# Kernel optimization log

Measured on AMD Instinct MI355X. Metric: run time of the kernel, lower is better.

Reference implementation:

```python
import jax, jax.numpy as jnp
import numpy as np

N_NODES = 20000
N_EDGES = 640000
D_IN = 128
D_OUT = 128


def setup_inputs() -> dict:
    key = jax.random.key(0)
    k1, k2, k3, k4 = jax.random.split(key, 4)
    x = jax.random.normal(k1, (N_NODES, D_IN), dtype=jnp.float32)
    edge_index = jax.random.randint(k2, (2, N_EDGES), 0, N_NODES, dtype=jnp.int64)
    edge_weight = jnp.ones((N_EDGES,), dtype=jnp.float32)
    # Linear(in_feats, out_feats) params (PyTorch convention: W [out, in])
    bound = 1.0 / np.sqrt(D_IN)
    W = jax.random.uniform(k3, (D_OUT, D_IN), minval=-bound, maxval=bound, dtype=jnp.float32)
    b = jax.random.uniform(k4, (D_OUT,), minval=-bound, maxval=bound, dtype=jnp.float32)
    return {"x": x, "edge_index": edge_index, "edge_weight": edge_weight, "W": W, "b": b}


def reference(x, edge_index, edge_weight, W, b):
    # MeanAggregator: h = Linear(x); out = row-normalized spmm(adj, h)
    h = x @ W.T + b  # [N, D_OUT]
    row, col = edge_index[0], edge_index[1]
    # message = w_ij * h[j], scattered into row i  (spmm with COO adjacency)
    msg = h[col] * edge_weight[:, None]  # [E, D_OUT]
    agg = jax.ops.segment_sum(msg, row, num_segments=N_NODES)  # [N, D_OUT]
    deg = jax.ops.segment_sum(edge_weight, row, num_segments=N_NODES)  # [N]
    deg_inv = jnp.where(deg > 0, 1.0 / deg, 0.0)
    out = agg * deg_inv[:, None]
    # normalize=True -> F.normalize(out, p=2, dim=-1)
    norm = jnp.linalg.norm(out, axis=-1, keepdims=True)
    out = out / jnp.maximum(norm, 1e-12)
    return out
```

## Files before the change

### kernel.cpp

```cpp
#include <hip/hip_runtime.h>
#include <hip/hip_bf16.h>
#include <math.h>

#define N_NODES 20000
#define N_EDGES 640000
#define D 128

#define BSHIFT 4
#define BNODES 16
#define NB 1250
#define CAP2 768
#define AGG_T 1024
#define NBLK1 160
#define CHUNK 4000
#define GPAD 16
#define CASTBLK 625

#define GROWS 16

typedef __attribute__((ext_vector_type(8))) short bf16x8;
typedef __attribute__((ext_vector_type(4))) float f32x4;

static __device__ __forceinline__ unsigned short f2bf(float f) {
  unsigned u = __float_as_uint(f);
  return (unsigned short)((u + 0x7fffu + ((u >> 16) & 1u)) >> 16);
}
static __device__ __forceinline__ float bflo(unsigned v) {
  return __uint_as_float(v << 16);
}
static __device__ __forceinline__ float bfhi(unsigned v) {
  return __uint_as_float(v & 0xffff0000u);
}

__global__ __launch_bounds__(256) void zero_kernel(int* __restrict__ p, int n) {
  const int i = blockIdx.x * 256 + threadIdx.x;
  if (i < n) p[i] = 0;
}

__global__ __launch_bounds__(AGG_T) void castbin_kernel(
    const float* __restrict__ x, const float* __restrict__ W,
    const int* __restrict__ rows, const int* __restrict__ cols,
    const float* __restrict__ ew,
    unsigned* __restrict__ xb, unsigned* __restrict__ Wb,
    int* __restrict__ gcur, uint2* __restrict__ bins) {
  __shared__ uint2 stage[CHUNK];
  __shared__ int cnt[NB];
  __shared__ int lbase[NB];
  __shared__ int gbase[NB];
  const int tid = threadIdx.x;
  if (blockIdx.x < NBLK1) {
    const int e0 = blockIdx.x * CHUNK;
    for (int i = tid; i < NB; i += AGG_T) cnt[i] = 0;
    __syncthreads();
    const int4* r4 = reinterpret_cast<const int4*>(rows + e0);
    int4 rv;
    const bool own = tid < CHUNK / 4;
    if (own) {
      rv = r4[tid];
      atomicAdd(&cnt[rv.x >> BSHIFT], 1);
      atomicAdd(&cnt[rv.y >> BSHIFT], 1);
      atomicAdd(&cnt[rv.z >> BSHIFT], 1);
      atomicAdd(&cnt[rv.w >> BSHIFT], 1);
    }
    __syncthreads();
    if (tid < 64) {
      int carry = 0;
      for (int c0 = 0; c0 < NB; c0 += 64) {
        const int idx = c0 + tid;
        const int v = (idx < NB) ? cnt[idx] : 0;
        int s = v;
#pragma unroll
        for (int off = 1; off < 64; off <<= 1) {
          const int t = __shfl_up(s, off);
          if (tid >= off) s += t;
        }
        if (idx < NB) lbase[idx] = carry + s - v;
        carry += __shfl(s, 63);
      }
    }
    for (int i = tid; i < NB; i += AGG_T) {
      const int c = cnt[i];
      gbase[i] = c ? atomicAdd(&gcur[i * GPAD], c) : 0;
    }
    __syncthreads();
    for (int i = tid; i < NB; i += AGG_T) cnt[i] = 0;
    __syncthreads();
    if (own) {
      const int4 cv = reinterpret_cast<const int4*>(cols + e0)[tid];
      const float4 wv = reinterpret_cast<const float4*>(ew + e0)[tid];
      const int rr[4] = {rv.x, rv.y, rv.z, rv.w};
      const int cc[4] = {cv.x, cv.y, cv.z, cv.w};
      const float ww[4] = {wv.x, wv.y, wv.z, wv.w};
#pragma unroll
      for (int u = 0; u < 4; ++u) {
        const int b = rr[u] >> BSHIFT;
        const int r = atomicAdd(&cnt[b], 1);
        stage[lbase[b] + r] =
            make_uint2(((unsigned)rr[u] << 16) | (unsigned)cc[u],
                       __float_as_uint(ww[u]));
      }
    }
    __syncthreads();
    for (int i = tid; i < CHUNK; i += AGG_T) {
      const uint2 e = stage[i];
      const int b = (int)(e.x >> 20);
      const int p = gbase[b] + (i - lbase[b]);
      if (p < CAP2) bins[(size_t)b * CAP2 + p] = e;
    }
  } else {
    const int i = (blockIdx.x - NBLK1) * AGG_T + tid;
    {
      const float4 v = *reinterpret_cast<const float4*>(&x[(size_t)i * 4]);
      uint2 o;
      o.x = (unsigned)f2bf(v.x) | ((unsigned)f2bf(v.y) << 16);
      o.y = (unsigned)f2bf(v.z) | ((unsigned)f2bf(v.w) << 16);
      *reinterpret_cast<uint2*>(&xb[(size_t)i * 2]) = o;
    }
    if (i < D * D / 4) {
      const float4 v = *reinterpret_cast<const float4*>(&W[(size_t)i * 4]);
      uint2 o;
      o.x = (unsigned)f2bf(v.x) | ((unsigned)f2bf(v.y) << 16);
      o.y = (unsigned)f2bf(v.z) | ((unsigned)f2bf(v.w) << 16);
      *reinterpret_cast<uint2*>(&Wb[(size_t)i * 2]) = o;
    }
  }
}

__global__ __launch_bounds__(AGG_T, 8) void agg_gemm_kernel(
    const unsigned* __restrict__ xb, const int* __restrict__ gcur,
    const uint2* __restrict__ bins, const unsigned* __restrict__ Wb,
    const float* __restrict__ bias, float* __restrict__ out) {
  __shared__ uint2 list[CAP2];
  __shared__ unsigned aggls[BNODES * 64];
  __shared__ int cnt[BNODES];
  __shared__ int base[BNODES];
  __shared__ float degls[BNODES];
  const int b = blockIdx.x;
  const int tid = threadIdx.x;
  const int n = min(gcur[b * GPAD], CAP2);
  if (tid < BNODES) cnt[tid] = 0;
  __syncthreads();

  uint2 ev;
  int rk = -1, rl = 0;
  if (tid < n) {
    ev = bins[(size_t)b * CAP2 + tid];
    rl = (int)(ev.x >> 16) & 15;
    rk = atomicAdd(&cnt[rl], 1);
  }
  __syncthreads();
  if (tid < 64) {
    const int c = (tid < BNODES) ? cnt[tid] : 0;
    int s = c;
#pragma unroll
    for (int off = 1; off < BNODES; off <<= 1) {
      const int t = __shfl_up(s, off);
      if (tid >= off) s += t;
    }
    if (tid < BNODES) base[tid] = s - c;
  }
  __syncthreads();
  if (rk >= 0) list[base[rl] + rk] = ev;
  __syncthreads();

  const int wv = tid >> 6, lane = tid & 63;
  const int q4 = lane >> 4, fidx = lane & 15;
  {
    const int s = base[wv];
    const int ke = s + cnt[wv];
    float a[8] = {0.f, 0.f, 0.f, 0.f, 0.f, 0.f, 0.f, 0.f};
    float dw = 0.f;
    for (int k = s; k < ke; k += 32) {
      uint4 v[8];
      float w[8];
#pragma unroll
      for (int u = 0; u < 8; ++u) {
        int idx = k + u * 4 + q4;
        const bool ok = idx < ke;
        if (!ok) idx = ke - 1;
        const uint2 e = list[idx];
        w[u] = ok ? __uint_as_float(e.y) : 0.f;
        v[u] = *reinterpret_cast<const uint4*>(
            &xb[(size_t)(e.x & 0xffffu) * (D / 2) + fidx * 4]);
      }
#pragma unroll
      for (int u = 0; u < 8; ++u) {
        a[0] += bflo(v[u].x) * w[u]; a[1] += bfhi(v[u].x) * w[u];
        a[2] += bflo(v[u].y) * w[u]; a[3] += bfhi(v[u].y) * w[u];
        a[4] += bflo(v[u].z) * w[u]; a[5] += bfhi(v[u].z) * w[u];
        a[6] += bflo(v[u].w) * w[u]; a[7] += bfhi(v[u].w) * w[u];
        dw += w[u];
      }
    }
#pragma unroll
    for (int j = 0; j < 8; ++j) {
      a[j] += __shfl_xor(a[j], 16);
      a[j] += __shfl_xor(a[j], 32);
    }
    dw += __shfl_xor(dw, 16);
    dw += __shfl_xor(dw, 32);
    const float dinv = dw > 0.f ? 1.f / dw : 0.f;
    if (lane == 0) degls[wv] = dw;
    if (q4 == 0) {
      uint4 o;
      o.x = (unsigned)f2bf(a[0] * dinv) | ((unsigned)f2bf(a[1] * dinv) << 16);
      o.y = (unsigned)f2bf(a[2] * dinv) | ((unsigned)f2bf(a[3] * dinv) << 16);
      o.z = (unsigned)f2bf(a[4] * dinv) | ((unsigned)f2bf(a[5] * dinv) << 16);
      o.w = (unsigned)f2bf(a[6] * dinv) | ((unsigned)f2bf(a[7] * dinv) << 16);
      *reinterpret_cast<uint4*>(
          &aggls[wv * 64 + ((fidx * 4) ^ ((wv & 7) << 2))]) = o;
    }
  }
  __syncthreads();

  if (wv != 0) return;
  const int arow = lane & 15;
  const int koff = (lane >> 4) * 4;

  bf16x8 afr[4];
#pragma unroll
  for (int kk = 0; kk < 4; ++kk) {
    const int wbase = (kk * 16 + koff) ^ ((arow & 7) << 2);
    union { uint4 u; bf16x8 v; } cv;
    cv.u = *reinterpret_cast<const uint4*>(&aggls[arow * 64 + wbase]);
    afr[kk] = cv.v;
  }

  f32x4 acc[8];
#pragma unroll
  for (int t = 0; t < 8; ++t) {
    const int o = t * 16 + (lane & 15);
    f32x4 c = {0.f, 0.f, 0.f, 0.f};
#pragma unroll
    for (int kk = 0; kk < 4; ++kk) {
      union { uint4 u; bf16x8 v; } cv;
      cv.u = *reinterpret_cast<const uint4*>(
          &Wb[(size_t)o * (D / 2) + kk * 16 + koff]);
      c = __builtin_amdgcn_mfma_f32_16x16x32_bf16(afr[kk], cv.v, c, 0, 0, 0);
    }
    acc[t] = c;
  }

  float ss[4] = {0.f, 0.f, 0.f, 0.f};
#pragma unroll
  for (int t = 0; t < 8; ++t) {
    const float bc = bias[t * 16 + (lane & 15)];
#pragma unroll
    for (int r = 0; r < 4; ++r) {
      const float y = acc[t][r] + bc;
      acc[t][r] = y;
      ss[r] += y * y;
    }
  }
#pragma unroll
  for (int r = 0; r < 4; ++r) {
#pragma unroll
    for (int off = 1; off < 16; off <<= 1)
      ss[r] += __shfl_xor(ss[r], off);
  }
  const int row0 = b * BNODES;
  float scale[4];
#pragma unroll
  for (int r = 0; r < 4; ++r) {
    const int lrow = (lane >> 4) * 4 + r;
    const float dw = degls[lrow];
    scale[r] = (dw > 0.f) ? 1.f / fmaxf(sqrtf(ss[r]), 1e-12f) : 0.f;
  }
#pragma unroll
  for (int t = 0; t < 8; ++t) {
#pragma unroll
    for (int r = 0; r < 4; ++r) {
      const int lrow = (lane >> 4) * 4 + r;
      out[(size_t)(row0 + lrow) * D + t * 16 + (lane & 15)] =
          acc[t][r] * scale[r];
    }
  }
}

__global__ __launch_bounds__(256) void scatter_kernel(
    const float* __restrict__ x, const int* __restrict__ rows,
    const int* __restrict__ cols, const float* __restrict__ ew,
    float* __restrict__ out, float* __restrict__ degw) {
  const int e = blockIdx.x * 4 + (threadIdx.x >> 6);
  const int lane = threadIdx.x & 63;
  if (e >= N_EDGES) return;
  const int r = rows[e];
  const int c = cols[e];
  const float w = ew[e];
  const float2 v = *reinterpret_cast<const float2*>(&x[(size_t)c * D + lane * 2]);
  atomicAdd(&out[(size_t)r * D + lane * 2], v.x * w);
  atomicAdd(&out[(size_t)r * D + lane * 2 + 1], v.y * w);
  if (lane == 0) atomicAdd(&degw[r], w);
}

__global__ __launch_bounds__(256) void linear_norm_kernel(
    const float* __restrict__ W, const float* __restrict__ b,
    const float* __restrict__ degw, float* __restrict__ out) {
  __shared__ float Ws[D][D + 1];
  __shared__ float xs[GROWS][D];
  __shared__ float dws[GROWS];
  const int tid = threadIdx.x;
  const int row0 = blockIdx.x * GROWS;
  for (int idx = tid; idx < D * D; idx += 256)
    Ws[idx >> 7][idx & 127] = W[idx];
  if (tid < GROWS) dws[tid] = degw[row0 + tid];
  __syncthreads();
  for (int idx = tid; idx < GROWS * D; idx += 256) {
    const int r = idx >> 7;
    const float dw = dws[r];
    const float dinv = dw > 0.f ? 1.f / dw : 0.f;
    xs[r][idx & 127] = out[(size_t)(row0 + r) * D + (idx & 127)] * dinv;
  }
  __syncthreads();
  const int o = tid & 127;
  const int rh = tid >> 7;
  float acc[GROWS / 2];
#pragma unroll
  for (int j = 0; j < GROWS / 2; ++j) acc[j] = 0.f;
  for (int k = 0; k < D; ++k) {
    const float wv = Ws[o][k];
#pragma unroll
    for (int j = 0; j < GROWS / 2; ++j)
      acc[j] += xs[rh + 2 * j][k] * wv;
  }
  const float bias = b[o];
  __syncthreads();
#pragma unroll
  for (int j = 0; j < GROWS / 2; ++j)
    xs[rh + 2 * j][o] = acc[j] + bias;
  __syncthreads();
  const int w = tid >> 6, lane = tid & 63;
#pragma unroll
  for (int q = 0; q < 4; ++q) {
    const int r = w * 4 + q;
    const float2 v = *reinterpret_cast<const float2*>(&xs[r][lane * 2]);
    float ss = v.x * v.x + v.y * v.y;
#pragma unroll
    for (int off = 1; off < 64; off <<= 1) ss += __shfl_xor(ss, off);
    const float dw = dws[r];
    const float scale = (dw > 0.f) ? 1.f / fmaxf(sqrtf(ss), 1e-12f) : 0.f;
    *reinterpret_cast<float2*>(&out[(size_t)(row0 + r) * D + lane * 2]) =
        make_float2(v.x * scale, v.y * scale);
  }
}

extern "C" void kernel_launch(void* const* d_in, const int* in_sizes, int n_in,
                              void* d_out, int out_size, void* d_ws, size_t ws_size,
                              hipStream_t stream) {
  const float* x  = (const float*)d_in[0];
  const int*   ei = (const int*)d_in[1];
  const float* ew = (const float*)d_in[2];
  const float* W  = (const float*)d_in[3];
  const float* b  = (const float*)d_in[4];
  float* out = (float*)d_out;
  char* ws = (char*)d_ws;

  const int* rows = ei;
  const int* cols = ei + N_EDGES;

  size_t off = 0;
  int* gcur = (int*)(ws + off);        off += (size_t)NB * GPAD * 4;
  float* degw = (float*)(ws + off);    off += (size_t)N_NODES * 4;
  unsigned* xb = (unsigned*)(ws + off);  off += (size_t)N_NODES * (D / 2) * 4;
  unsigned* Wb = (unsigned*)(ws + off);  off += (size_t)D * (D / 2) * 4;
  uint2* bins = (uint2*)(ws + off);    off += (size_t)NB * CAP2 * 8;
  const size_t main_bytes = off;
  const size_t fallback_bytes = (size_t)NB * GPAD * 4 + (size_t)N_NODES * 4;

  if (ws_size >= main_bytes) {
    zero_kernel<<<(NB * GPAD + 255) / 256, 256, 0, stream>>>(gcur, NB * GPAD);
    castbin_kernel<<<NBLK1 + CASTBLK, AGG_T, 0, stream>>>(x, W, rows, cols, ew,
                                                          xb, Wb, gcur, bins);
    agg_gemm_kernel<<<NB, AGG_T, 0, stream>>>(xb, gcur, bins, Wb, b, out);
  } else if (ws_size >= fallback_bytes) {
    hipMemsetAsync(out, 0, (size_t)N_NODES * D * 4, stream);
    hipMemsetAsync(degw, 0, (size_t)N_NODES * 4, stream);
    scatter_kernel<<<(N_EDGES + 3) / 4, 256, 0, stream>>>(x, rows, cols, ew, out, degw);
    linear_norm_kernel<<<N_NODES / GROWS, 256, 0, stream>>>(W, b, degw, out);
  }
}
```

Baseline: 64.27 us.

## Split feature gather into low/high halves across two kernels for cache locality

After: 73.29 us. 14.0% more time.

```diff
diff --git a/kernel.cpp b/kernel.cpp
--- a/kernel.cpp
+++ b/kernel.cpp
@@ -41,7 +41,8 @@
     const float* __restrict__ x, const float* __restrict__ W,
     const int* __restrict__ rows, const int* __restrict__ cols,
     const float* __restrict__ ew,
-    unsigned* __restrict__ xb, unsigned* __restrict__ Wb,
+    unsigned* __restrict__ xb_lo, unsigned* __restrict__ xb_hi,
+    unsigned* __restrict__ Wb,
     int* __restrict__ gcur, uint2* __restrict__ bins) {
   __shared__ uint2 stage[CHUNK];
   __shared__ int cnt[NB];
@@ -110,11 +111,16 @@
   } else {
     const int i = (blockIdx.x - NBLK1) * AGG_T + tid;
     {
+      const int node = i >> 5;
+      const int q = i & 31;
       const float4 v = *reinterpret_cast<const float4*>(&x[(size_t)i * 4]);
       uint2 o;
       o.x = (unsigned)f2bf(v.x) | ((unsigned)f2bf(v.y) << 16);
       o.y = (unsigned)f2bf(v.z) | ((unsigned)f2bf(v.w) << 16);
-      *reinterpret_cast<uint2*>(&xb[(size_t)i * 2]) = o;
+      unsigned* dst = (q < 16)
+          ? &xb_lo[(size_t)node * 32 + q * 2]
+          : &xb_hi[(size_t)node * 32 + (q - 16) * 2];
+      *reinterpret_cast<uint2*>(dst) = o;
     }
     if (i < D * D / 4) {
       const float4 v = *reinterpret_cast<const float4*>(&W[(size_t)i * 4]);
@@ -126,10 +132,93 @@
   }
 }
 
-__global__ __launch_bounds__(AGG_T, 8) void agg_gemm_kernel(
-    const unsigned* __restrict__ xb, const int* __restrict__ gcur,
-    const uint2* __restrict__ bins, const unsigned* __restrict__ Wb,
-    const float* __restrict__ bias, float* __restrict__ out) {
+__global__ __launch_bounds__(AGG_T) void agg_lo_kernel(
+    const unsigned* __restrict__ xb_lo, const int* __restrict__ gcur,
+    const uint2* __restrict__ bins, unsigned* __restrict__ aggb_lo) {
+  __shared__ uint2 list[CAP2];
+  __shared__ int cnt[BNODES];
+  __shared__ int base[BNODES];
+  const int b = blockIdx.x;
+  const int tid = threadIdx.x;
+  const int n = min(gcur[b * GPAD], CAP2);
+  if (tid < BNODES) cnt[tid] = 0;
+  __syncthreads();
+  uint2 ev;
+  int rk = -1, rl = 0;
+  if (tid < n) {
+    ev = bins[(size_t)b * CAP2 + tid];
+    rl = (int)(ev.x >> 16) & 15;
+    rk = atomicAdd(&cnt[rl], 1);
+  }
+  __syncthreads();
+  if (tid < 64) {
+    const int c = (tid < BNODES) ? cnt[tid] : 0;
+    int s = c;
+#pragma unroll
+    for (int off = 1; off < BNODES; off <<= 1) {
+      const int t = __shfl_up(s, off);
+      if (tid >= off) s += t;
+    }
+    if (tid < BNODES) base[tid] = s - c;
+  }
+  __syncthreads();
+  if (rk >= 0) list[base[rl] + rk] = ev;
+  __syncthreads();
+
+  const int wv = tid >> 6, lane = tid & 63;
+  const int o8 = lane >> 3, f = lane & 7;
+  const int s = base[wv];
+  const int ke = s + cnt[wv];
+  float a[8] = {0.f, 0.f, 0.f, 0.f, 0.f, 0.f, 0.f, 0.f};
+  float dw = 0.f;
+  for (int k = s; k < ke; k += 64) {
+    uint4 v[8];
+    float w[8];
+#pragma unroll
+    for (int u = 0; u < 8; ++u) {
+      int idx = k + u * 8 + o8;
+      const bool ok = idx < ke;
+      if (!ok) idx = ke - 1;
+      const uint2 e = list[idx];
+      w[u] = ok ? __uint_as_float(e.y) : 0.f;
+      v[u] = *reinterpret_cast<const uint4*>(
+          &xb_lo[(size_t)(e.x & 0xffffu) * 32 + f * 4]);
+    }
+#pragma unroll
+    for (int u = 0; u < 8; ++u) {
+      a[0] += bflo(v[u].x) * w[u]; a[1] += bfhi(v[u].x) * w[u];
+      a[2] += bflo(v[u].y) * w[u]; a[3] += bfhi(v[u].y) * w[u];
+      a[4] += bflo(v[u].z) * w[u]; a[5] += bfhi(v[u].z) * w[u];
+      a[6] += bflo(v[u].w) * w[u]; a[7] += bfhi(v[u].w) * w[u];
+      dw += w[u];
+    }
+  }
+#pragma unroll
+  for (int j = 0; j < 8; ++j) {
+    a[j] += __shfl_xor(a[j], 8);
+    a[j] += __shfl_xor(a[j], 16);
+    a[j] += __shfl_xor(a[j], 32);
+  }
+  dw += __shfl_xor(dw, 8);
+  dw += __shfl_xor(dw, 16);
+  dw += __shfl_xor(dw, 32);
+  const float dinv = dw > 0.f ? 1.f / dw : 0.f;
+  if (lane < 8) {
+    uint4 o;
+    o.x = (unsigned)f2bf(a[0] * dinv) | ((unsigned)f2bf(a[1] * dinv) << 16);
+    o.y = (unsigned)f2bf(a[2] * dinv) | ((unsigned)f2bf(a[3] * dinv) << 16);
+    o.z = (unsigned)f2bf(a[4] * dinv) | ((unsigned)f2bf(a[5] * dinv) << 16);
+    o.w = (unsigned)f2bf(a[6] * dinv) | ((unsigned)f2bf(a[7] * dinv) << 16);
+    *reinterpret_cast<uint4*>(
+        &aggb_lo[(size_t)(b * BNODES + wv) * 32 + f * 4]) = o;
+  }
+}
+
+__global__ __launch_bounds__(AGG_T) void agg_hi_gemm_kernel(
+    const unsigned* __restrict__ xb_hi, const int* __restrict__ gcur,
+    const uint2* __restrict__ bins, const unsigned* __restrict__ aggb_lo,
+    const unsigned* __restrict__ Wb, const float* __restrict__ bias,
+    float* __restrict__ out) {
   __shared__ uint2 list[CAP2];
   __shared__ unsigned aggls[BNODES * 64];
   __shared__ int cnt[BNODES];
@@ -140,7 +229,6 @@
   const int n = min(gcur[b * GPAD], CAP2);
   if (tid < BNODES) cnt[tid] = 0;
   __syncthreads();
-
   uint2 ev;
   int rk = -1, rl = 0;
   if (tid < n) {
@@ -161,27 +249,34 @@
   }
   __syncthreads();
   if (rk >= 0) list[base[rl] + rk] = ev;
+  if (tid < BNODES * 8) {
+    const int node = tid >> 3, f = tid & 7;
+    const uint4 cv = *reinterpret_cast<const uint4*>(
+        &aggb_lo[(size_t)(b * BNODES + node) * 32 + f * 4]);
+    *reinterpret_cast<uint4*>(
+        &aggls[node * 64 + ((f * 4) ^ ((node & 7) << 2))]) = cv;
+  }
   __syncthreads();
 
   const int wv = tid >> 6, lane = tid & 63;
-  const int q4 = lane >> 4, fidx = lane & 15;
+  const int o8 = lane >> 3, f = lane & 7;
   {
     const int s = base[wv];
     const int ke = s + cnt[wv];
     float a[8] = {0.f, 0.f, 0.f, 0.f, 0.f, 0.f, 0.f, 0.f};
     float dw = 0.f;
-    for (int k = s; k < ke; k += 32) {
+    for (int k = s; k < ke; k += 64) {
       uint4 v[8];
       float w[8];
 #pragma unroll
       for (int u = 0; u < 8; ++u) {
-        int idx = k + u * 4 + q4;
+        int idx = k + u * 8 + o8;
         const bool ok = idx < ke;
         if (!ok) idx = ke - 1;
         const uint2 e = list[idx];
         w[u] = ok ? __uint_as_float(e.y) : 0.f;
         v[u] = *reinterpret_cast<const uint4*>(
-            &xb[(size_t)(e.x & 0xffffu) * (D / 2) + fidx * 4]);
+            &xb_hi[(size_t)(e.x & 0xffffu) * 32 + f * 4]);
       }
 #pragma unroll
       for (int u = 0; u < 8; ++u) {
@@ -194,21 +289,23 @@
     }
 #pragma unroll
     for (int j = 0; j < 8; ++j) {
+      a[j] += __shfl_xor(a[j], 8);
       a[j] += __shfl_xor(a[j], 16);
       a[j] += __shfl_xor(a[j], 32);
     }
+    dw += __shfl_xor(dw, 8);
     dw += __shfl_xor(dw, 16);
     dw += __shfl_xor(dw, 32);
     const float dinv = dw > 0.f ? 1.f / dw : 0.f;
     if (lane == 0) degls[wv] = dw;
-    if (q4 == 0) {
+    if (lane < 8) {
       uint4 o;
       o.x = (unsigned)f2bf(a[0] * dinv) | ((unsigned)f2bf(a[1] * dinv) << 16);
       o.y = (unsigned)f2bf(a[2] * dinv) | ((unsigned)f2bf(a[3] * dinv) << 16);
       o.z = (unsigned)f2bf(a[4] * dinv) | ((unsigned)f2bf(a[5] * dinv) << 16);
       o.w = (unsigned)f2bf(a[6] * dinv) | ((unsigned)f2bf(a[7] * dinv) << 16);
       *reinterpret_cast<uint4*>(
-          &aggls[wv * 64 + ((fidx * 4) ^ ((wv & 7) << 2))]) = o;
+          &aggls[wv * 64 + ((32 + f * 4) ^ ((wv & 7) << 2))]) = o;
     }
   }
   __syncthreads();
@@ -359,19 +456,23 @@
   const int* cols = ei + N_EDGES;
 
   size_t off = 0;
-  int* gcur = (int*)(ws + off);        off += (size_t)NB * GPAD * 4;
-  float* degw = (float*)(ws + off);    off += (size_t)N_NODES * 4;
-  unsigned* xb = (unsigned*)(ws + off);  off += (size_t)N_NODES * (D / 2) * 4;
+  int* gcur = (int*)(ws + off);          off += (size_t)NB * GPAD * 4;
+  float* degw = (float*)(ws + off);      off += (size_t)N_NODES * 4;
+  unsigned* xb_lo = (unsigned*)(ws + off);  off += (size_t)N_NODES * 32 * 4;
+  unsigned* xb_hi = (unsigned*)(ws + off);  off += (size_t)N_NODES * 32 * 4;
+  unsigned* aggb_lo = (unsigned*)(ws + off); off += (size_t)N_NODES * 32 * 4;
   unsigned* Wb = (unsigned*)(ws + off);  off += (size_t)D * (D / 2) * 4;
-  uint2* bins = (uint2*)(ws + off);    off += (size_t)NB * CAP2 * 8;
+  uint2* bins = (uint2*)(ws + off);      off += (size_t)NB * CAP2 * 8;
   const size_t main_bytes = off;
   const size_t fallback_bytes = (size_t)NB * GPAD * 4 + (size_t)N_NODES * 4;
 
   if (ws_size >= main_bytes) {
     zero_kernel<<<(NB * GPAD + 255) / 256, 256, 0, stream>>>(gcur, NB * GPAD);
-    castbin_kernel<<<NBLK1 + CASTBLK, AGG_T, 0, stream>>>(x, W, rows, cols, ew,
-                                                          xb, Wb, gcur, bins);
-    agg_gemm_kernel<<<NB, AGG_T, 0, stream>>>(xb, gcur, bins, Wb, b, out);
+    castbin_kernel<<<NBLK1 + CASTBLK, AGG_T, 0, stream>>>(
+        x, W, rows, cols, ew, xb_lo, xb_hi, Wb, gcur, bins);
+    agg_lo_kernel<<<NB, AGG_T, 0, stream>>>(xb_lo, gcur, bins, aggb_lo);
+    agg_hi_gemm_kernel<<<NB, AGG_T, 0, stream>>>(xb_hi, gcur, bins, aggb_lo,
+                                                 Wb, b, out);
   } else if (ws_size >= fallback_bytes) {
     hipMemsetAsync(out, 0, (size_t)N_NODES * D * 4, stream);
     hipMemsetAsync(degw, 0, (size_t)N_NODES * 4, stream);
```
